# Optimization experiments

Hardware: AMD Instinct MI355X
Metric: run time of the kernel (lower is better)

## Reference

```python
import jax, jax.numpy as jnp
import numpy as np

B = 8192      # batch size
D = 512       # feature dim == num_classes (centers is [C, C] in the original)
C = 512       # num_classes
MARGIN = 1.0


def setup_inputs() -> dict:
    key = jax.random.key(0)
    k1, k2, k3 = jax.random.split(key, 3)
    inputs = jax.random.normal(k1, (B, D), dtype=jnp.float32)
    targets = jax.random.randint(k2, (B,), 0, C)
    centers = jax.random.normal(k3, (C, D), dtype=jnp.float32)  # learned param
    return {"inputs": inputs, "targets": targets, "centers": centers}


def reference(inputs, targets, centers):
    # centers_batch[j] = centers[targets[j]]  (gather rows)
    cb = centers[targets]                                   # [B, D]
    # dist[i, j] = || inputs[i] - cb[j] ||_2, computed via the expanded form
    # (||a||^2 + ||b||^2 - 2 a.b) so we never materialize a [B, B, D] tensor.
    sq = ((inputs * inputs).sum(-1)[:, None]
          + (cb * cb).sum(-1)[None, :]
          - 2.0 * (inputs @ cb.T))                          # [B, B]
    dist = jnp.sqrt(jnp.clip(sq, 1e-12))                    # clamp(min=1e-12).sqrt()

    # mask[i, j] = (targets[i] == targets[j]); note original indexes dist[i][mask[i]]
    mask = targets[:, None] == targets[None, :]             # [B, B] bool
    dist_ap = jnp.max(jnp.where(mask, dist, -jnp.inf), axis=1)   # hardest positive per row
    dist_an = jnp.min(jnp.where(mask, jnp.inf, dist), axis=1)    # hardest negative per row

    # MarginRankingLoss(margin)(dist_an, dist_ap, y=1) = mean(relu(dist_ap - dist_an + margin))
    loss = jnp.mean(jnp.maximum(0.0, dist_ap - dist_an + MARGIN))
    prec = jnp.mean((dist_an > dist_ap).astype(jnp.float32))
    return loss, prec
```

## Files before the change

kernel.cpp:

```cpp
#include <hip/hip_runtime.h>
#include <hip/hip_bf16.h>

#define NB 8192
#define ND 512
#define NC 512
#define MARGIN_F 1.0f
#define BIGF 3.0e38f

typedef __attribute__((ext_vector_type(8))) short bf16x8;
typedef __attribute__((ext_vector_type(4))) float f32x4;

__device__ __forceinline__ unsigned fkey(float f) {
    unsigned u = __float_as_uint(f);
    unsigned mask = (u & 0x80000000u) ? 0xFFFFFFFFu : 0x80000000u;
    return u ^ mask;
}
__device__ __forceinline__ float finv(unsigned k) {
    unsigned mask = (k & 0x80000000u) ? 0x80000000u : 0xFFFFFFFFu;
    return __uint_as_float(k ^ mask);
}
__device__ __forceinline__ unsigned short f2bf(float f) {
    __hip_bfloat16 h = __float2bfloat16(f);
    return __builtin_bit_cast(unsigned short, h);
}

#define GLOAD_LDS16(g, l)                                                    \
    __builtin_amdgcn_global_load_lds(                                        \
        (const __attribute__((address_space(1))) void*)(g),                  \
        (__attribute__((address_space(3))) void*)(l), 16, 0, 0)

__global__ __launch_bounds__(256) void k0_prep(
    const float* __restrict__ inputs, const int* __restrict__ targets,
    const float* __restrict__ centers,
    unsigned short* __restrict__ inB, unsigned short* __restrict__ cenB,
    float* __restrict__ rsq, float* __restrict__ csq,
    unsigned* __restrict__ counts, unsigned* __restrict__ anG,
    unsigned* __restrict__ ctrl, unsigned long long* __restrict__ acc2)
{
    const int bid = blockIdx.x;
    const int tid = threadIdx.x;

    if (bid == 2176) {
        __shared__ unsigned hist[NC];
        if (tid < 65) ctrl[tid] = 0u;
        if (tid == 65) { acc2[0] = 0ull; acc2[1] = 0ull; }
        for (int i = tid; i < NC; i += 256) hist[i] = 0u;
        __syncthreads();
        for (int i = tid; i < NB; i += 256) atomicAdd(&hist[targets[i]], 1u);
        __syncthreads();
        for (int i = tid; i < NC; i += 256) counts[i] = hist[i];
        return;
    }

    const int wave = tid >> 6, lane = tid & 63;
    const float* src;
    unsigned short* dst;
    float* sqdst;
    int row;
    bool is_input = (bid < 2048);
    if (is_input) {
        row   = bid * 4 + wave;
        src   = inputs + (size_t)row * ND;
        dst   = inB + (size_t)row * ND;
        sqdst = rsq + row;
        if (tid < 4) anG[bid * 4 + tid] = 0xFFFFFFFFu;
    } else {
        row   = (bid - 2048) * 4 + wave;
        src   = centers + (size_t)row * ND;
        dst   = cenB + (size_t)row * ND;
        sqdst = csq + row;
    }

    float4 v1 = ((const float4*)src)[lane];
    float4 v2 = ((const float4*)src)[lane + 64];
    float s = v1.x*v1.x + v1.y*v1.y + v1.z*v1.z + v1.w*v1.w
            + v2.x*v2.x + v2.y*v2.y + v2.z*v2.z + v2.w*v2.w;

    ushort4 o1, o2;
    o1.x = f2bf(v1.x); o1.y = f2bf(v1.y); o1.z = f2bf(v1.z); o1.w = f2bf(v1.w);
    o2.x = f2bf(v2.x); o2.y = f2bf(v2.y); o2.z = f2bf(v2.z); o2.w = f2bf(v2.w);
    ((ushort4*)dst)[lane]      = o1;
    ((ushort4*)dst)[lane + 64] = o2;

    #pragma unroll
    for (int off = 32; off > 0; off >>= 1) s += __shfl_down(s, off);
    if (lane == 0) *sqdst = s;
}

__global__ __launch_bounds__(256) void k2_mfma(
    const unsigned short* __restrict__ Ain, const unsigned short* __restrict__ cenB,
    const int* __restrict__ targets, const unsigned* __restrict__ counts,
    const float* __restrict__ csq, const float* __restrict__ rsq,
    unsigned* __restrict__ anG, float* __restrict__ apG,
    unsigned* __restrict__ ctrl, unsigned long long* __restrict__ acc2,
    float* __restrict__ out)
{
    __shared__ __align__(16) unsigned short As[2][128 * 32];
    __shared__ __align__(16) unsigned short Bs[2][64 * 32];
    __shared__ int      tgtL[128];
    __shared__ float    csqL[64];
    __shared__ unsigned ldsmin[128];
    __shared__ double   fa[4], fp_[4];
    __shared__ int      isfin;

    const int tid  = threadIdx.x;
    const int w    = tid >> 6;
    const int lane = tid & 63;
    const int wm   = w >> 1;
    const int wn   = w & 1;
    const int qd   = lane >> 4;
    const int ln   = lane & 15;

    const int bid   = blockIdx.x;
    const int rt    = bid & 63;
    const int rbase = rt * 128;
    const int ct    = bid >> 6;
    const int cbase = ct * 64;

    if (tid < 128) { tgtL[tid] = targets[rbase + tid]; ldsmin[tid] = 0xFFFFFFFFu; }
    if (tid < 64) {
        const int c = cbase + tid;
        csqL[tid] = (counts[c] > 0u) ? csq[c] : BIGF;
    }

    const int arow0 = w * 32 + (lane >> 2);
    const int brow  = w * 16 + (lane >> 2);
    const int scol  = (lane & 3) * 8;
    const unsigned short* gA0 = Ain  + (size_t)(rbase + arow0)      * ND + scol;
    const unsigned short* gA1 = Ain  + (size_t)(rbase + arow0 + 16) * ND + scol;
    const unsigned short* gB  = cenB + (size_t)(cbase + brow)       * ND + scol;

    f32x4 acc[4][2] = {};

#define STAGE(buf, kb) do {                                                  \
        GLOAD_LDS16(gA0 + (kb), &As[buf][(w * 32)      * 32]);               \
        GLOAD_LDS16(gA1 + (kb), &As[buf][(w * 32 + 16) * 32]);               \
        GLOAD_LDS16(gB  + (kb), &Bs[buf][(w * 16)      * 32]);               \
    } while (0)

#define COMPUTE(buf) do {                                                    \
        bf16x8 a[4], b[2];                                                   \
        _Pragma("unroll")                                                    \
        for (int i = 0; i < 4; ++i)                                          \
            a[i] = *(const bf16x8*)&As[buf][(wm * 64 + i * 16 + ln) * 32 + qd * 8]; \
        _Pragma("unroll")                                                    \
        for (int j = 0; j < 2; ++j)                                          \
            b[j] = *(const bf16x8*)&Bs[buf][(wn * 32 + j * 16 + ln) * 32 + qd * 8]; \
        _Pragma("unroll")                                                    \
        for (int i = 0; i < 4; ++i)                                          \
            _Pragma("unroll")                                                \
            for (int j = 0; j < 2; ++j)                                      \
                acc[i][j] = __builtin_amdgcn_mfma_f32_16x16x32_bf16(a[i], b[j], acc[i][j], 0, 0, 0); \
    } while (0)

    STAGE(0, 0);
    __syncthreads();
    int cur = 0;
    #pragma unroll
    for (int kb = 32; kb < ND; kb += 32) {
        STAGE(cur ^ 1, kb);
        COMPUTE(cur);
        __syncthreads();
        cur ^= 1;
    }
    COMPUTE(cur);

    #pragma unroll
    for (int i = 0; i < 4; ++i) {
        #pragma unroll
        for (int r = 0; r < 4; ++r) {
            const int rlocal = wm * 64 + i * 16 + qd * 4 + r;
            const int grow   = rbase + rlocal;
            const int tr     = tgtL[rlocal];
            float m = BIGF;
            #pragma unroll
            for (int j = 0; j < 2; ++j) {
                const int clocal = wn * 32 + j * 16 + ln;
                const float val = csqL[clocal] - 2.0f * acc[i][j][r];
                if (cbase + clocal == tr) {
                    atomicExch((unsigned*)apG + grow, __float_as_uint(val));
                } else {
                    m = fminf(m, val);
                }
            }
            #pragma unroll
            for (int off = 1; off < 16; off <<= 1)
                m = fminf(m, __shfl_xor(m, off));
            if (ln == 0) atomicMin(&ldsmin[rlocal], fkey(m));
        }
    }
    __syncthreads();
    if (tid < 128)
        atomicMin(&anG[rbase + tid], ldsmin[tid]);
    __syncthreads();

    if (tid == 0)
        isfin = (atomicAdd(&ctrl[rt], 1u) == 7u) ? 1 : 0;
    __syncthreads();
    if (!isfin) return;

    double a = 0.0, p = 0.0;
    if (tid < 128) {
        const int r = rbase + tid;
        const unsigned ank = atomicMin(&anG[r], 0xFFFFFFFFu);
        const unsigned apu = atomicOr((unsigned*)apG + r, 0u);
        const float mv  = finv(ank);
        const float apv = __uint_as_float(apu);
        const float s   = rsq[r];
        const float an  = sqrtf(fmaxf(s + mv,  1e-12f));
        const float ap  = sqrtf(fmaxf(s + apv, 1e-12f));
        a = (double)fmaxf(0.0f, ap - an + MARGIN_F);
        p = (an > ap) ? 1.0 : 0.0;
    }
    #pragma unroll
    for (int off = 32; off > 0; off >>= 1) {
        a += __shfl_down(a, off);
        p += __shfl_down(p, off);
    }
    if (lane == 0) { fa[w] = a; fp_[w] = p; }
    __syncthreads();
    if (tid == 0) {
        const double A = fa[0] + fa[1] + fa[2] + fa[3];
        const double P = fp_[0] + fp_[1] + fp_[2] + fp_[3];
        atomicAdd(&acc2[0], (unsigned long long)(A * 4294967296.0 + 0.5));
        atomicAdd(&acc2[1], (unsigned long long)(P + 0.5));
        asm volatile("s_waitcnt vmcnt(0)" ::: "memory");
        if (atomicAdd(&ctrl[64], 1u) == 63u) {
            unsigned long long ls = atomicAdd(&acc2[0], 0ull);
            unsigned long long ps = atomicAdd(&acc2[1], 0ull);
            out[0] = (float)((double)ls / (4294967296.0 * (double)NB));
            out[1] = (float)((double)ps / (double)NB);
        }
    }
}

extern "C" void kernel_launch(void* const* d_in, const int* in_sizes, int n_in,
                              void* d_out, int out_size, void* d_ws, size_t ws_size,
                              hipStream_t stream) {
    const float* inputs  = (const float*)d_in[0];
    const int*   targets = (const int*)d_in[1];
    const float* centers = (const float*)d_in[2];
    float* out = (float*)d_out;

    char* wp = (char*)d_ws;
    unsigned short* inB    = (unsigned short*)(wp);
    unsigned short* cenB   = (unsigned short*)(wp + 8388608);
    float*          rsq    = (float*)(wp + 8912896);
    float*          csqv   = (float*)(wp + 8945664);
    unsigned*       counts = (unsigned*)(wp + 8947712);
    float*          apG    = (float*)(wp + 8949760);
    unsigned*       anG    = (unsigned*)(wp + 8982528);
    unsigned*       ctrl   = (unsigned*)(wp + 9015296);
    unsigned long long* acc2 = (unsigned long long*)(wp + 9015808);

    k0_prep<<<2177, 256, 0, stream>>>(inputs, targets, centers,
                                      inB, cenB, rsq, csqv, counts,
                                      anG, ctrl, acc2);
    k2_mfma<<<512, 256, 0, stream>>>(inB, cenB, targets, counts, csqv, rsq,
                                     anG, apG, ctrl, acc2, out);
}
```

Measured before the change: 92.29 us.

## Fuse input bf16 conversion and row norms into the MFMA kernel

The prep kernel now converts only the centers. Each GEMM block loads fp32 input rows straight into registers, computes their squared norms, converts them to bf16, and writes them into a swizzled LDS layout. This removes the separate input conversion pass and its bf16 round trip through global memory. In exchange, each of the 8 column-tile blocks re-reads fp32 inputs (twice the bytes of bf16) and redoes the conversion. The A operand also loses the asynchronous global-to-LDS load path.

New measurement: 94.83 us. 2.8% more time.

```diff
diff --git a/kernel.cpp b/kernel.cpp
--- a/kernel.cpp
+++ b/kernel.cpp
@@ -8,6 +8,7 @@
 #define BIGF 3.0e38f
 
 typedef __attribute__((ext_vector_type(8))) short bf16x8;
+typedef __attribute__((ext_vector_type(8))) unsigned short u16x8;
 typedef __attribute__((ext_vector_type(4))) float f32x4;
 
 __device__ __forceinline__ unsigned fkey(float f) {
@@ -29,18 +30,16 @@
         (const __attribute__((address_space(1))) void*)(g),                  \
         (__attribute__((address_space(3))) void*)(l), 16, 0, 0)
 
-__global__ __launch_bounds__(256) void k0_prep(
-    const float* __restrict__ inputs, const int* __restrict__ targets,
-    const float* __restrict__ centers,
-    unsigned short* __restrict__ inB, unsigned short* __restrict__ cenB,
-    float* __restrict__ rsq, float* __restrict__ csq,
+__global__ __launch_bounds__(256) void k0c(
+    const float* __restrict__ centers, const int* __restrict__ targets,
+    unsigned short* __restrict__ cenB, float* __restrict__ csq,
     unsigned* __restrict__ counts, unsigned* __restrict__ anG,
     unsigned* __restrict__ ctrl, unsigned long long* __restrict__ acc2)
 {
     const int bid = blockIdx.x;
     const int tid = threadIdx.x;
 
-    if (bid == 2176) {
+    if (bid == 128) {
         __shared__ unsigned hist[NC];
         if (tid < 65) ctrl[tid] = 0u;
         if (tid == 65) { acc2[0] = 0ull; acc2[1] = 0ull; }
@@ -52,24 +51,12 @@
         return;
     }
 
+    if (tid < 64) anG[bid * 64 + tid] = 0xFFFFFFFFu;
+
     const int wave = tid >> 6, lane = tid & 63;
-    const float* src;
-    unsigned short* dst;
-    float* sqdst;
-    int row;
-    bool is_input = (bid < 2048);
-    if (is_input) {
-        row   = bid * 4 + wave;
-        src   = inputs + (size_t)row * ND;
-        dst   = inB + (size_t)row * ND;
-        sqdst = rsq + row;
-        if (tid < 4) anG[bid * 4 + tid] = 0xFFFFFFFFu;
-    } else {
-        row   = (bid - 2048) * 4 + wave;
-        src   = centers + (size_t)row * ND;
-        dst   = cenB + (size_t)row * ND;
-        sqdst = csq + row;
-    }
+    const int row = bid * 4 + wave;
+    const float* src = centers + (size_t)row * ND;
+    unsigned short* dst = cenB + (size_t)row * ND;
 
     float4 v1 = ((const float4*)src)[lane];
     float4 v2 = ((const float4*)src)[lane + 64];
@@ -84,13 +71,13 @@
 
     #pragma unroll
     for (int off = 32; off > 0; off >>= 1) s += __shfl_down(s, off);
-    if (lane == 0) *sqdst = s;
+    if (lane == 0) csq[row] = s;
 }
 
 __global__ __launch_bounds__(256) void k2_mfma(
-    const unsigned short* __restrict__ Ain, const unsigned short* __restrict__ cenB,
+    const float* __restrict__ inputs, const unsigned short* __restrict__ cenB,
     const int* __restrict__ targets, const unsigned* __restrict__ counts,
-    const float* __restrict__ csq, const float* __restrict__ rsq,
+    const float* __restrict__ csq,
     unsigned* __restrict__ anG, float* __restrict__ apG,
     unsigned* __restrict__ ctrl, unsigned long long* __restrict__ acc2,
     float* __restrict__ out)
@@ -100,6 +87,7 @@
     __shared__ int      tgtL[128];
     __shared__ float    csqL[64];
     __shared__ unsigned ldsmin[128];
+    __shared__ float    rsqL[128];
     __shared__ double   fa[4], fp_[4];
     __shared__ int      isfin;
 
@@ -123,26 +111,54 @@
         csqL[tid] = (counts[c] > 0u) ? csq[c] : BIGF;
     }
 
-    const int arow0 = w * 32 + (lane >> 2);
-    const int brow  = w * 16 + (lane >> 2);
-    const int scol  = (lane & 3) * 8;
-    const unsigned short* gA0 = Ain  + (size_t)(rbase + arow0)      * ND + scol;
-    const unsigned short* gA1 = Ain  + (size_t)(rbase + arow0 + 16) * ND + scol;
-    const unsigned short* gB  = cenB + (size_t)(cbase + brow)       * ND + scol;
+    const int brow = w * 16 + (lane >> 2);
+    const int scol = (lane & 3) * 8;
+    const unsigned short* gB = cenB + (size_t)(cbase + brow) * ND + scol;
+
+    const int ar  = tid >> 1;
+    const int ah  = tid & 1;
+    const float* gA = inputs + (size_t)(rbase + ar) * ND + ah * 16;
+    const int axr = (ar >> 1) & 3;
+    const int wb0 = ar * 64 + ((2 * ah + 0) ^ axr) * 16;
+    const int wb1 = ar * 64 + ((2 * ah + 1) ^ axr) * 16;
+
+    int aoff[4];
+    #pragma unroll
+    for (int i = 0; i < 4; ++i) {
+        const int rho = wm * 64 + i * 16 + ln;
+        aoff[i] = rho * 64 + ((qd ^ ((rho >> 1) & 3)) * 16);
+    }
 
     f32x4 acc[4][2] = {};
-
-#define STAGE(buf, kb) do {                                                  \
-        GLOAD_LDS16(gA0 + (kb), &As[buf][(w * 32)      * 32]);               \
-        GLOAD_LDS16(gA1 + (kb), &As[buf][(w * 32 + 16) * 32]);               \
-        GLOAD_LDS16(gB  + (kb), &Bs[buf][(w * 16)      * 32]);               \
+    float ss = 0.0f;
+    float4 A0, A1, A2, A3;
+
+#define LOADA(kb) do {                                                       \
+        const float4* ap_ = (const float4*)(gA + (kb));                      \
+        A0 = ap_[0]; A1 = ap_[1]; A2 = ap_[2]; A3 = ap_[3];                  \
     } while (0)
+
+#define CVTWR(buf) do {                                                      \
+        ss += A0.x*A0.x + A0.y*A0.y + A0.z*A0.z + A0.w*A0.w                  \
+            + A1.x*A1.x + A1.y*A1.y + A1.z*A1.z + A1.w*A1.w                  \
+            + A2.x*A2.x + A2.y*A2.y + A2.z*A2.z + A2.w*A2.w                  \
+            + A3.x*A3.x + A3.y*A3.y + A3.z*A3.z + A3.w*A3.w;                 \
+        u16x8 p0_, p1_;                                                      \
+        p0_[0]=f2bf(A0.x); p0_[1]=f2bf(A0.y); p0_[2]=f2bf(A0.z); p0_[3]=f2bf(A0.w); \
+        p0_[4]=f2bf(A1.x); p0_[5]=f2bf(A1.y); p0_[6]=f2bf(A1.z); p0_[7]=f2bf(A1.w); \
+        p1_[0]=f2bf(A2.x); p1_[1]=f2bf(A2.y); p1_[2]=f2bf(A2.z); p1_[3]=f2bf(A2.w); \
+        p1_[4]=f2bf(A3.x); p1_[5]=f2bf(A3.y); p1_[6]=f2bf(A3.z); p1_[7]=f2bf(A3.w); \
+        *(u16x8*)((char*)&As[buf][0] + wb0) = p0_;                           \
+        *(u16x8*)((char*)&As[buf][0] + wb1) = p1_;                           \
+    } while (0)
+
+#define STAGE_B(buf, kb) GLOAD_LDS16(gB + (kb), &Bs[buf][(w * 16) * 32])
 
 #define COMPUTE(buf) do {                                                    \
         bf16x8 a[4], b[2];                                                   \
         _Pragma("unroll")                                                    \
         for (int i = 0; i < 4; ++i)                                          \
-            a[i] = *(const bf16x8*)&As[buf][(wm * 64 + i * 16 + ln) * 32 + qd * 8]; \
+            a[i] = *(const bf16x8*)((const char*)&As[buf][0] + aoff[i]);     \
         _Pragma("unroll")                                                    \
         for (int j = 0; j < 2; ++j)                                          \
             b[j] = *(const bf16x8*)&Bs[buf][(wn * 32 + j * 16 + ln) * 32 + qd * 8]; \
@@ -153,17 +169,24 @@
                 acc[i][j] = __builtin_amdgcn_mfma_f32_16x16x32_bf16(a[i], b[j], acc[i][j], 0, 0, 0); \
     } while (0)
 
-    STAGE(0, 0);
+    LOADA(0);
+    STAGE_B(0, 0);
+    CVTWR(0);
     __syncthreads();
     int cur = 0;
     #pragma unroll
     for (int kb = 32; kb < ND; kb += 32) {
-        STAGE(cur ^ 1, kb);
+        LOADA(kb);
+        STAGE_B(cur ^ 1, kb);
         COMPUTE(cur);
+        CVTWR(cur ^ 1);
         __syncthreads();
         cur ^= 1;
     }
     COMPUTE(cur);
+
+    ss += __shfl_xor(ss, 1);
+    if (ah == 0) rsqL[ar] = ss;
 
     #pragma unroll
     for (int i = 0; i < 4; ++i) {
@@ -206,7 +229,7 @@
         const unsigned apu = atomicOr((unsigned*)apG + r, 0u);
         const float mv  = finv(ank);
         const float apv = __uint_as_float(apu);
-        const float s   = rsq[r];
+        const float s   = rsqL[tid];
         const float an  = sqrtf(fmaxf(s + mv,  1e-12f));
         const float ap  = sqrtf(fmaxf(s + apv, 1e-12f));
         a = (double)fmaxf(0.0f, ap - an + MARGIN_F);
@@ -243,19 +266,16 @@
     float* out = (float*)d_out;
 
     char* wp = (char*)d_ws;
-    unsigned short* inB    = (unsigned short*)(wp);
-    unsigned short* cenB   = (unsigned short*)(wp + 8388608);
-    float*          rsq    = (float*)(wp + 8912896);
-    float*          csqv   = (float*)(wp + 8945664);
-    unsigned*       counts = (unsigned*)(wp + 8947712);
-    float*          apG    = (float*)(wp + 8949760);
-    unsigned*       anG    = (unsigned*)(wp + 8982528);
-    unsigned*       ctrl   = (unsigned*)(wp + 9015296);
-    unsigned long long* acc2 = (unsigned long long*)(wp + 9015808);
-
-    k0_prep<<<2177, 256, 0, stream>>>(inputs, targets, centers,
-                                      inB, cenB, rsq, csqv, counts,
-                                      anG, ctrl, acc2);
-    k2_mfma<<<512, 256, 0, stream>>>(inB, cenB, targets, counts, csqv, rsq,
+    unsigned short* cenB   = (unsigned short*)(wp);
+    float*          csqv   = (float*)(wp + 524288);
+    unsigned*       counts = (unsigned*)(wp + 526336);
+    float*          apG    = (float*)(wp + 528384);
+    unsigned*       anG    = (unsigned*)(wp + 561152);
+    unsigned*       ctrl   = (unsigned*)(wp + 593920);
+    unsigned long long* acc2 = (unsigned long long*)(wp + 594432);
+
+    k0c<<<129, 256, 0, stream>>>(centers, targets, cenB, csqv, counts,
+                                 anG, ctrl, acc2);
+    k2_mfma<<<512, 256, 0, stream>>>(inputs, cenB, targets, counts, csqv,
                                      anG, apG, ctrl, acc2, out);
 }
```
